# Performance work log

Hardware: AMD Instinct MI355X
Metric: run time of the kernel (lower is better)

## Reference

```python
import jax, jax.numpy as jnp
import numpy as np

N, C, SUBVEC, K, DOUT, DEPTH = 16384, 64, 16, 16, 1024, 4


def setup_inputs() -> dict:
    key = jax.random.key(0)
    k1, k2, k3, k4, k5 = jax.random.split(key, 5)
    x = jax.random.normal(k1, (N, C * SUBVEC), dtype=jnp.float32)
    split_idxs = jax.random.randint(k2, (C, DEPTH), 0, SUBVEC, dtype=jnp.int32)
    split_vals = jax.random.normal(k3, (C, DEPTH, K // 2), dtype=jnp.float32)
    lookup_tables = jax.random.normal(k4, (C, K, DOUT), dtype=jnp.float32)
    bias = jax.random.normal(k5, (DOUT,), dtype=jnp.float32)
    return {"x": x, "split_idxs": split_idxs, "split_vals": split_vals,
            "lookup_tables": lookup_tables, "bias": bias}


def _encode(x_sub, split_idxs, split_vals):
    # x_sub: (n, C, subvec_len); split_idxs: (C, 4); split_vals: (C, 4, 8)
    n = x_sub.shape[0]
    c_idx = jnp.arange(C)
    enc = jnp.zeros((n, C), dtype=jnp.int32)
    for t in range(DEPTH):  # fixed tree depth 4
        xv = x_sub[:, c_idx, split_idxs[:, t]]            # (n, C) selected feature per codebook
        thresh = split_vals[c_idx[None, :], t, enc]       # (n, C) per-node threshold
        enc = 2 * enc + (xv > thresh).astype(jnp.int32)
    return enc  # values in [0, 16)


def reference(x, split_idxs, split_vals, lookup_tables, bias):
    n = x.shape[0]
    x_sub = x.reshape(n, C, SUBVEC)
    enc = _encode(x_sub, split_idxs, split_vals)           # (n, C) int32
    onehot = jax.nn.one_hot(enc, K, dtype=x.dtype)         # (n, C, K)
    out = jnp.einsum('nck,cko->no', onehot, lookup_tables) # sum over codebooks of LUT rows
    return out + bias
```

## Files before the change

kernel.cpp:

```cpp
#include <hip/hip_runtime.h>

#define NN    16384
#define CBN   64
#define SUBV  16
#define KCODE 16
#define DOUTN 1024
#define DEP   4

typedef short bf16x8 __attribute__((ext_vector_type(8)));
typedef float f32x16 __attribute__((ext_vector_type(16)));

static __device__ __forceinline__ unsigned short f2bf(float f) {
  unsigned int u = __float_as_uint(f);
  u += 0x7FFFu + ((u >> 16) & 1u);
  return (unsigned short)(u >> 16);
}

static __device__ __forceinline__ void gld16(const void* g, void* l) {
  __builtin_amdgcn_global_load_lds(
      (const __attribute__((address_space(1))) unsigned int*)g,
      (__attribute__((address_space(3))) unsigned int*)(uintptr_t)l, 16, 0, 0);
}

__global__ __launch_bounds__(256) void prep_k(
    const float* __restrict__ x, const int* __restrict__ split_idxs,
    const float* __restrict__ split_vals, const float* __restrict__ Tg,
    unsigned char* __restrict__ codes, unsigned int* __restrict__ Tswz) {
  const int t = threadIdx.x;

  if (blockIdx.x < 64) {
    const int img = blockIdx.x;
    const int g = img >> 3, ch = img & 7;
    unsigned int* dst = Tswz + (size_t)img * 8192;
    const int colq = t & 31, kp = (t >> 5) & 7;
    #pragma unroll
    for (int cl = 0; cl < 8; ++cl) {
      const float* g0 = Tg + ((size_t)((ch * 8 + cl) * KCODE + 2 * kp)) * DOUTN
                        + g * 128 + colq * 4;
      float4 r0 = *(const float4*)g0;
      float4 r1 = *(const float4*)(g0 + DOUTN);
      unsigned int pk[4] = {
        f2bf(r0.x) | ((unsigned int)f2bf(r1.x) << 16),
        f2bf(r0.y) | ((unsigned int)f2bf(r1.y) << 16),
        f2bf(r0.z) | ((unsigned int)f2bf(r1.z) << 16),
        f2bf(r0.w) | ((unsigned int)f2bf(r1.w) << 16)};
      unsigned key = (unsigned)(colq & 7) << 2;
      #pragma unroll
      for (int j = 0; j < 4; ++j)
        dst[cl * 1024 + ((((unsigned)(colq * 4 + j)) * 8 + (unsigned)kp) ^ key)]
            = pk[j];
    }
    return;
  }

  __shared__ __align__(16) float xs[8][SUBV * CBN];
  __shared__ int   sidxT[DEP * CBN];
  __shared__ float svalT[DEP * (KCODE / 2) * CBN];
  if (t < DEP * CBN) {
    int d = t >> 6, c = t & 63;
    sidxT[t] = split_idxs[c * DEP + d];
  }
  for (int i = t; i < DEP * (KCODE / 2) * CBN; i += 256) {
    int c = i & 63, de = i >> 6, d = de >> 3, e = de & 7;
    svalT[i] = split_vals[(c * DEP + d) * (KCODE / 2) + e];
  }
  const int n0 = (blockIdx.x - 64) * 8;
  const float4* xg = (const float4*)(x + (size_t)n0 * DOUTN);
  #pragma unroll
  for (int i = 0; i < 8; ++i) {
    int li = t + i * 256;
    int r = li >> 8, cpos = li & 255;
    float4 v = xg[r * 256 + cpos];
    int c = cpos >> 2, q = cpos & 3;
    *(float4*)&xs[r][c * SUBV + ((q ^ (c & 3)) << 2)] = v;
  }
  __syncthreads();
  const int c = t & 63, rg = t >> 6;
  #pragma unroll
  for (int i = 0; i < 2; ++i) {
    int nl = rg * 2 + i;
    int e = 0;
    #pragma unroll
    for (int d = 0; d < DEP; ++d) {
      int si = sidxT[d * 64 + c];
      float xv = xs[nl][c * SUBV + (((si >> 2) ^ (c & 3)) << 2) + (si & 3)];
      float th = svalT[(d * 8 + e) * 64 + c];
      e = 2 * e + (xv > th ? 1 : 0);
    }
    codes[(size_t)(n0 + nl) * CBN + c] = (unsigned char)e;
  }
}

__global__ __launch_bounds__(1024, 4) void maddness_mfma(
    const unsigned int* __restrict__ Tswz, const float* __restrict__ bias,
    const unsigned char* __restrict__ codes, float* __restrict__ out) {
  __shared__ __align__(16) unsigned int Tb[32768];

  const int t = threadIdx.x;
  const int wid = t >> 6, lane = t & 63, lrow = lane & 31, h = lane >> 5;
  const int g16 = blockIdx.x, g8 = g16 >> 1, half = g16 & 1;
  const int n0 = blockIdx.y * 1024;
  const char* img = (const char*)Tswz + (size_t)g8 * 8 * 32768;

  #pragma unroll
  for (int i = 0; i < 8; ++i) {
    int gs = wid * 8 + i;
    int ch = gs >> 4, s16 = gs & 15, cl = s16 >> 1, pc = s16 & 1;
    gld16(img + ch * 32768 + cl * 4096 + half * 2048 + pc * 1024 + lane * 16,
          (char*)Tb + gs * 1024);
  }

  f32x16 acc[2][2];
  #pragma unroll
  for (int rt = 0; rt < 2; ++rt)
    #pragma unroll
    for (int ct = 0; ct < 2; ++ct)
      #pragma unroll
      for (int e = 0; e < 16; ++e) acc[rt][ct][e] = 0.f;

  const unsigned char* crow0 = codes + (size_t)(n0 + wid * 64 + lrow) * CBN;
  const unsigned char* crow1 = crow0 + 32 * CBN;

  __syncthreads();

  #pragma unroll
  for (int ct = 0; ct < 2; ++ct) {
    const unsigned col_loc = (unsigned)(ct * 32 + lrow);
    const unsigned rb = (col_loc * 16 + (unsigned)h * 8)
                      ^ (((col_loc >> 2) & 7u) << 3);
    const unsigned short* tb0 = (const unsigned short*)Tb + rb;

    #pragma unroll
    for (int i = 0; i < 8; ++i) {
      const int ch = (wid + i) & 7;
      const unsigned long long qw0 = *(const unsigned long long*)(crow0 + ch * 8);
      const unsigned long long qw1 = *(const unsigned long long*)(crow1 + ch * 8);
      const unsigned short* tbc = tb0 + ch * 8192;

      bf16x8 bva[4], bvb[4];
      #pragma unroll
      for (int k = 0; k < 4; ++k)
        bva[k] = *(const bf16x8*)(tbc + k * 1024);

      #pragma unroll
      for (int hb = 0; hb < 2; ++hb) {
        if (hb == 0) {
          #pragma unroll
          for (int k = 0; k < 4; ++k)
            bvb[k] = *(const bf16x8*)(tbc + (4 + k) * 1024);
        }
        #pragma unroll
        for (int k = 0; k < 4; ++k) {
          const int cl = hb * 4 + k;
          const bf16x8 bv = hb ? bvb[k] : bva[k];
          #pragma unroll
          for (int rt = 0; rt < 2; ++rt) {
            const unsigned long long q = rt ? qw1 : qw0;
            int c = (int)((q >> (8 * cl)) & 255);
            int p = c >> 1;
            unsigned s = 0x3F80u << ((c & 1) << 4);
            union { unsigned int u[4]; bf16x8 v; } A;
            #pragma unroll
            for (int j = 0; j < 4; ++j) A.u[j] = (p == h * 4 + j) ? s : 0u;
            acc[rt][ct] = __builtin_amdgcn_mfma_f32_32x32x16_bf16(A.v, bv, acc[rt][ct], 0, 0, 0);
          }
        }
      }
    }
  }

  #pragma unroll
  for (int ct = 0; ct < 2; ++ct) {
    const int col = g16 * 64 + ct * 32 + lrow;
    const float bval = bias[col];
    #pragma unroll
    for (int rt = 0; rt < 2; ++rt)
      #pragma unroll
      for (int r = 0; r < 16; ++r) {
        int row = n0 + wid * 64 + rt * 32 + (r & 3) + 8 * (r >> 2) + 4 * h;
        out[(size_t)row * DOUTN + col] = acc[rt][ct][r] + bval;
      }
  }
}

extern "C" void kernel_launch(void* const* d_in, const int* in_sizes, int n_in,
                              void* d_out, int out_size, void* d_ws, size_t ws_size,
                              hipStream_t stream) {
  const float* x    = (const float*)d_in[0];
  const int*   sidx = (const int*)d_in[1];
  const float* sval = (const float*)d_in[2];
  const float* Tg   = (const float*)d_in[3];
  const float* bias = (const float*)d_in[4];
  float* out = (float*)d_out;
  unsigned char* codes = (unsigned char*)d_ws;
  unsigned int*  Tswz  = (unsigned int*)((char*)d_ws + (1 << 20));

  prep_k<<<64 + NN / 8, 256, 0, stream>>>(x, sidx, sval, Tg, codes, Tswz);
  maddness_mfma<<<dim3(16, 16), 1024, 0, stream>>>(Tswz, bias, codes, out);
}
```

Baseline: 52.51 us.

## Remap waves to 128x32 output tiles to reuse each LUT fragment across four MFMAs

Each wave previously computed a 64x64 tile (2 row tiles x 2 column tiles), loading its B fragments from LDS twice, once per column tile. Now each wave owns a 128-row by 32-column tile, loads each bf16 LUT fragment once, and reuses it across four row tiles. This halves the LDS reads of B per wave, at the cost of four code-row global loads per chunk instead of two. Each output store now covers one 32-wide column instead of two.

After: 59.48 us. 1.13x slower.

```diff
diff --git a/kernel.cpp b/kernel.cpp
--- a/kernel.cpp
+++ b/kernel.cpp
@@ -98,6 +98,7 @@
 
   const int t = threadIdx.x;
   const int wid = t >> 6, lane = t & 63, lrow = lane & 31, h = lane >> 5;
+  const int rq = wid >> 1, cq = wid & 1;
   const int g16 = blockIdx.x, g8 = g16 >> 1, half = g16 & 1;
   const int n0 = blockIdx.y * 1024;
   const char* img = (const char*)Tswz + (size_t)g8 * 8 * 32768;
@@ -110,77 +111,54 @@
           (char*)Tb + gs * 1024);
   }
 
-  f32x16 acc[2][2];
+  f32x16 acc[4];
   #pragma unroll
-  for (int rt = 0; rt < 2; ++rt)
+  for (int rt = 0; rt < 4; ++rt)
     #pragma unroll
-    for (int ct = 0; ct < 2; ++ct)
-      #pragma unroll
-      for (int e = 0; e < 16; ++e) acc[rt][ct][e] = 0.f;
+    for (int e = 0; e < 16; ++e) acc[rt][e] = 0.f;
 
-  const unsigned char* crow0 = codes + (size_t)(n0 + wid * 64 + lrow) * CBN;
-  const unsigned char* crow1 = crow0 + 32 * CBN;
+  const unsigned char* crow = codes + (size_t)(n0 + rq * 128 + lrow) * CBN;
+
+  const unsigned col_loc = (unsigned)(cq * 32 + lrow);
+  const unsigned rb = (col_loc * 16 + (unsigned)h * 8)
+                    ^ (((col_loc >> 2) & 7u) << 3);
+  const unsigned short* tb0 = (const unsigned short*)Tb + rb;
 
   __syncthreads();
 
   #pragma unroll
-  for (int ct = 0; ct < 2; ++ct) {
-    const unsigned col_loc = (unsigned)(ct * 32 + lrow);
-    const unsigned rb = (col_loc * 16 + (unsigned)h * 8)
-                      ^ (((col_loc >> 2) & 7u) << 3);
-    const unsigned short* tb0 = (const unsigned short*)Tb + rb;
-
+  for (int i = 0; i < 8; ++i) {
+    const int ch = (wid + i) & 7;
+    unsigned long long qw[4];
     #pragma unroll
-    for (int i = 0; i < 8; ++i) {
-      const int ch = (wid + i) & 7;
-      const unsigned long long qw0 = *(const unsigned long long*)(crow0 + ch * 8);
-      const unsigned long long qw1 = *(const unsigned long long*)(crow1 + ch * 8);
-      const unsigned short* tbc = tb0 + ch * 8192;
-
-      bf16x8 bva[4], bvb[4];
+    for (int rt = 0; rt < 4; ++rt)
+      qw[rt] = *(const unsigned long long*)(crow + (size_t)rt * 32 * CBN + ch * 8);
+    const unsigned short* tbc = tb0 + ch * 8192;
+    #pragma unroll
+    for (int cl = 0; cl < 8; ++cl) {
+      const bf16x8 bv = *(const bf16x8*)(tbc + cl * 1024);
       #pragma unroll
-      for (int k = 0; k < 4; ++k)
-        bva[k] = *(const bf16x8*)(tbc + k * 1024);
-
-      #pragma unroll
-      for (int hb = 0; hb < 2; ++hb) {
-        if (hb == 0) {
-          #pragma unroll
-          for (int k = 0; k < 4; ++k)
-            bvb[k] = *(const bf16x8*)(tbc + (4 + k) * 1024);
-        }
+      for (int rt = 0; rt < 4; ++rt) {
+        int c = (int)((qw[rt] >> (8 * cl)) & 255);
+        int p = c >> 1;
+        unsigned s = 0x3F80u << ((c & 1) << 4);
+        union { unsigned int u[4]; bf16x8 v; } A;
         #pragma unroll
-        for (int k = 0; k < 4; ++k) {
-          const int cl = hb * 4 + k;
-          const bf16x8 bv = hb ? bvb[k] : bva[k];
-          #pragma unroll
-          for (int rt = 0; rt < 2; ++rt) {
-            const unsigned long long q = rt ? qw1 : qw0;
-            int c = (int)((q >> (8 * cl)) & 255);
-            int p = c >> 1;
-            unsigned s = 0x3F80u << ((c & 1) << 4);
-            union { unsigned int u[4]; bf16x8 v; } A;
-            #pragma unroll
-            for (int j = 0; j < 4; ++j) A.u[j] = (p == h * 4 + j) ? s : 0u;
-            acc[rt][ct] = __builtin_amdgcn_mfma_f32_32x32x16_bf16(A.v, bv, acc[rt][ct], 0, 0, 0);
-          }
-        }
+        for (int j = 0; j < 4; ++j) A.u[j] = (p == h * 4 + j) ? s : 0u;
+        acc[rt] = __builtin_amdgcn_mfma_f32_32x32x16_bf16(A.v, bv, acc[rt], 0, 0, 0);
       }
     }
   }
 
+  const int col = g16 * 64 + cq * 32 + lrow;
+  const float bval = bias[col];
   #pragma unroll
-  for (int ct = 0; ct < 2; ++ct) {
-    const int col = g16 * 64 + ct * 32 + lrow;
-    const float bval = bias[col];
+  for (int rt = 0; rt < 4; ++rt)
     #pragma unroll
-    for (int rt = 0; rt < 2; ++rt)
-      #pragma unroll
-      for (int r = 0; r < 16; ++r) {
-        int row = n0 + wid * 64 + rt * 32 + (r & 3) + 8 * (r >> 2) + 4 * h;
-        out[(size_t)row * DOUTN + col] = acc[rt][ct][r] + bval;
-      }
-  }
+    for (int r = 0; r < 16; ++r) {
+      int row = n0 + rq * 128 + rt * 32 + (r & 3) + 8 * (r >> 2) + 4 * h;
+      out[(size_t)row * DOUTN + col] = acc[rt][r] + bval;
+    }
 }
 
 extern "C" void kernel_launch(void* const* d_in, const int* in_sizes, int n_in,
```

## Quantize lookup tables to int8 with per-column scales and use i8 MFMA

Applied to the files above, without the earlier changes.

Replaces the bf16 lookup-table image and bf16 MFMA with int8-quantized tables, using a per-output-column absmax scale, and int32-accumulating 32x32x32 i8 MFMA. The scale is applied in the epilogue with an fma alongside the bias. This halves LDS footprint and table traffic and doubles K per MFMA, cutting the instruction count. Int8 quantization adds much more error than bf16 and may break tolerance. The prep kernel also gains a column-max reduction pass.

After: 46.68 us. -11.1%, faster.

```diff
diff --git a/kernel.cpp b/kernel.cpp
--- a/kernel.cpp
+++ b/kernel.cpp
@@ -7,14 +7,8 @@
 #define DOUTN 1024
 #define DEP   4
 
-typedef short bf16x8 __attribute__((ext_vector_type(8)));
-typedef float f32x16 __attribute__((ext_vector_type(16)));
-
-static __device__ __forceinline__ unsigned short f2bf(float f) {
-  unsigned int u = __float_as_uint(f);
-  u += 0x7FFFu + ((u >> 16) & 1u);
-  return (unsigned short)(u >> 16);
-}
+typedef int   i32x4  __attribute__((ext_vector_type(4)));
+typedef int   i32x16 __attribute__((ext_vector_type(16)));
 
 static __device__ __forceinline__ void gld16(const void* g, void* l) {
   __builtin_amdgcn_global_load_lds(
@@ -25,30 +19,52 @@
 __global__ __launch_bounds__(256) void prep_k(
     const float* __restrict__ x, const int* __restrict__ split_idxs,
     const float* __restrict__ split_vals, const float* __restrict__ Tg,
-    unsigned char* __restrict__ codes, unsigned int* __restrict__ Tswz) {
+    unsigned char* __restrict__ codes, unsigned char* __restrict__ img,
+    float* __restrict__ scales) {
   const int t = threadIdx.x;
 
   if (blockIdx.x < 64) {
-    const int img = blockIdx.x;
-    const int g = img >> 3, ch = img & 7;
-    unsigned int* dst = Tswz + (size_t)img * 8192;
-    const int colq = t & 31, kp = (t >> 5) & 7;
-    #pragma unroll
-    for (int cl = 0; cl < 8; ++cl) {
-      const float* g0 = Tg + ((size_t)((ch * 8 + cl) * KCODE + 2 * kp)) * DOUTN
-                        + g * 128 + colq * 4;
-      float4 r0 = *(const float4*)g0;
-      float4 r1 = *(const float4*)(g0 + DOUTN);
-      unsigned int pk[4] = {
-        f2bf(r0.x) | ((unsigned int)f2bf(r1.x) << 16),
-        f2bf(r0.y) | ((unsigned int)f2bf(r1.y) << 16),
-        f2bf(r0.z) | ((unsigned int)f2bf(r1.z) << 16),
-        f2bf(r0.w) | ((unsigned int)f2bf(r1.w) << 16)};
-      unsigned key = (unsigned)(colq & 7) << 2;
-      #pragma unroll
-      for (int j = 0; j < 4; ++j)
-        dst[cl * 1024 + ((((unsigned)(colq * 4 + j)) * 8 + (unsigned)kp) ^ key)]
-            = pk[j];
+    __shared__ float pm[16][17];
+    __shared__ float invs[16];
+    const int col0 = blockIdx.x * 16;
+    const int j = t & 15, rg = t >> 4;
+    float m = 0.f;
+    for (int r = rg; r < 1024; r += 16)
+      m = fmaxf(m, fabsf(Tg[(size_t)r * DOUTN + col0 + j]));
+    pm[rg][j] = m;
+    __syncthreads();
+    if (t < 16) {
+      float mm = 0.f;
+      #pragma unroll
+      for (int k = 0; k < 16; ++k) mm = fmaxf(mm, pm[k][t]);
+      scales[col0 + t] = mm * (1.f / 127.f);
+      invs[t] = 127.f / mm;
+    }
+    __syncthreads();
+    #pragma unroll
+    for (int ii = 0; ii < 4; ++ii) {
+      int u = t + ii * 256;
+      int p = u >> 5, h = (u >> 4) & 1, jj = u & 15;
+      int c = 2 * p + h;
+      int col = col0 + jj;
+      const float* src = Tg + (size_t)c * KCODE * DOUTN + col;
+      const float inv = invs[jj];
+      unsigned int pk[4];
+      #pragma unroll
+      for (int q = 0; q < 4; ++q) {
+        unsigned int w = 0;
+        #pragma unroll
+        for (int b = 0; b < 4; ++b) {
+          float v = src[(size_t)(q * 4 + b) * DOUTN];
+          float r = rintf(v * inv);
+          r = fminf(127.f, fmaxf(-127.f, r));
+          w |= ((unsigned int)((int)r & 255)) << (8 * b);
+        }
+        pk[q] = w;
+      }
+      unsigned int* dst = (unsigned int*)(img + ((size_t)(col >> 6)) * 65536
+                                          + p * 2048 + h * 1024 + (col & 63) * 16);
+      dst[0] = pk[0]; dst[1] = pk[1]; dst[2] = pk[2]; dst[3] = pk[3];
     }
     return;
   }
@@ -75,10 +91,10 @@
     *(float4*)&xs[r][c * SUBV + ((q ^ (c & 3)) << 2)] = v;
   }
   __syncthreads();
-  const int c = t & 63, rg = t >> 6;
+  const int c = t & 63, rg2 = t >> 6;
   #pragma unroll
   for (int i = 0; i < 2; ++i) {
-    int nl = rg * 2 + i;
+    int nl = rg2 * 2 + i;
     int e = 0;
     #pragma unroll
     for (int d = 0; d < DEP; ++d) {
@@ -92,79 +108,66 @@
 }
 
 __global__ __launch_bounds__(1024, 4) void maddness_mfma(
-    const unsigned int* __restrict__ Tswz, const float* __restrict__ bias,
-    const unsigned char* __restrict__ codes, float* __restrict__ out) {
-  __shared__ __align__(16) unsigned int Tb[32768];
+    const unsigned char* __restrict__ img, const float* __restrict__ scales,
+    const float* __restrict__ bias, const unsigned char* __restrict__ codes,
+    float* __restrict__ out) {
+  __shared__ __align__(16) unsigned int Tb[16384];
 
   const int t = threadIdx.x;
   const int wid = t >> 6, lane = t & 63, lrow = lane & 31, h = lane >> 5;
-  const int g16 = blockIdx.x, g8 = g16 >> 1, half = g16 & 1;
+  const int g16 = blockIdx.x;
   const int n0 = blockIdx.y * 1024;
-  const char* img = (const char*)Tswz + (size_t)g8 * 8 * 32768;
-
-  #pragma unroll
-  for (int i = 0; i < 8; ++i) {
-    int gs = wid * 8 + i;
-    int ch = gs >> 4, s16 = gs & 15, cl = s16 >> 1, pc = s16 & 1;
-    gld16(img + ch * 32768 + cl * 4096 + half * 2048 + pc * 1024 + lane * 16,
-          (char*)Tb + gs * 1024);
-  }
-
-  f32x16 acc[2][2];
+  const unsigned char* img_g = img + (size_t)g16 * 65536;
+
+  #pragma unroll
+  for (int i = 0; i < 4; ++i) {
+    int gs = wid * 4 + i;
+    gld16(img_g + gs * 1024 + lane * 16, (char*)Tb + gs * 1024);
+  }
+
+  i32x16 acc[2][2];
   #pragma unroll
   for (int rt = 0; rt < 2; ++rt)
     #pragma unroll
     for (int ct = 0; ct < 2; ++ct)
       #pragma unroll
-      for (int e = 0; e < 16; ++e) acc[rt][ct][e] = 0.f;
+      for (int e = 0; e < 16; ++e) acc[rt][ct][e] = 0;
 
   const unsigned char* crow0 = codes + (size_t)(n0 + wid * 64 + lrow) * CBN;
   const unsigned char* crow1 = crow0 + 32 * CBN;
+  const char* tb = (const char*)Tb;
 
   __syncthreads();
 
-  #pragma unroll
-  for (int ct = 0; ct < 2; ++ct) {
-    const unsigned col_loc = (unsigned)(ct * 32 + lrow);
-    const unsigned rb = (col_loc * 16 + (unsigned)h * 8)
-                      ^ (((col_loc >> 2) & 7u) << 3);
-    const unsigned short* tb0 = (const unsigned short*)Tb + rb;
-
-    #pragma unroll
-    for (int i = 0; i < 8; ++i) {
-      const int ch = (wid + i) & 7;
-      const unsigned long long qw0 = *(const unsigned long long*)(crow0 + ch * 8);
-      const unsigned long long qw1 = *(const unsigned long long*)(crow1 + ch * 8);
-      const unsigned short* tbc = tb0 + ch * 8192;
-
-      bf16x8 bva[4], bvb[4];
-      #pragma unroll
-      for (int k = 0; k < 4; ++k)
-        bva[k] = *(const bf16x8*)(tbc + k * 1024);
-
-      #pragma unroll
-      for (int hb = 0; hb < 2; ++hb) {
-        if (hb == 0) {
-          #pragma unroll
-          for (int k = 0; k < 4; ++k)
-            bvb[k] = *(const bf16x8*)(tbc + (4 + k) * 1024);
-        }
-        #pragma unroll
-        for (int k = 0; k < 4; ++k) {
-          const int cl = hb * 4 + k;
-          const bf16x8 bv = hb ? bvb[k] : bva[k];
-          #pragma unroll
-          for (int rt = 0; rt < 2; ++rt) {
-            const unsigned long long q = rt ? qw1 : qw0;
-            int c = (int)((q >> (8 * cl)) & 255);
-            int p = c >> 1;
-            unsigned s = 0x3F80u << ((c & 1) << 4);
-            union { unsigned int u[4]; bf16x8 v; } A;
-            #pragma unroll
-            for (int j = 0; j < 4; ++j) A.u[j] = (p == h * 4 + j) ? s : 0u;
-            acc[rt][ct] = __builtin_amdgcn_mfma_f32_32x32x16_bf16(A.v, bv, acc[rt][ct], 0, 0, 0);
-          }
-        }
+  const int gg0 = wid & 7;
+  unsigned long long qA0 = *(const unsigned long long*)(crow0 + gg0 * 8);
+  unsigned long long qA1 = *(const unsigned long long*)(crow1 + gg0 * 8);
+
+  #pragma unroll
+  for (int g = 0; g < 8; ++g) {
+    const int gcur = (wid + g) & 7;
+    const unsigned long long q0 = qA0, q1 = qA1;
+    if (g < 7) {
+      const int ggn = (wid + g + 1) & 7;
+      qA0 = *(const unsigned long long*)(crow0 + ggn * 8);
+      qA1 = *(const unsigned long long*)(crow1 + ggn * 8);
+    }
+    #pragma unroll
+    for (int pp = 0; pp < 4; ++pp) {
+      const int p = gcur * 4 + pp;
+      const char* pb = tb + p * 2048 + h * 1024 + lrow * 16;
+      const i32x4 b0 = *(const i32x4*)pb;
+      const i32x4 b1 = *(const i32x4*)(pb + 512);
+      const unsigned sh = (unsigned)((pp * 2 + h) * 8);
+      #pragma unroll
+      for (int rt = 0; rt < 2; ++rt) {
+        const unsigned c4 = (unsigned)((rt ? q1 : q0) >> sh) & 15u;
+        const unsigned long long tt = 1ULL << ((c4 & 7u) * 8u);
+        union { unsigned long long q[2]; i32x4 v; } A;
+        A.q[0] = (c4 < 8u) ? tt : 0ULL;
+        A.q[1] = (c4 < 8u) ? 0ULL : tt;
+        acc[rt][0] = __builtin_amdgcn_mfma_i32_32x32x32_i8(A.v, b0, acc[rt][0], 0, 0, 0);
+        acc[rt][1] = __builtin_amdgcn_mfma_i32_32x32x32_i8(A.v, b1, acc[rt][1], 0, 0, 0);
       }
     }
   }
@@ -172,13 +175,14 @@
   #pragma unroll
   for (int ct = 0; ct < 2; ++ct) {
     const int col = g16 * 64 + ct * 32 + lrow;
-    const float bval = bias[col];
+    const float sc = scales[col];
+    const float bv = bias[col];
     #pragma unroll
     for (int rt = 0; rt < 2; ++rt)
       #pragma unroll
       for (int r = 0; r < 16; ++r) {
         int row = n0 + wid * 64 + rt * 32 + (r & 3) + 8 * (r >> 2) + 4 * h;
-        out[(size_t)row * DOUTN + col] = acc[rt][ct][r] + bval;
+        out[(size_t)row * DOUTN + col] = fmaf((float)acc[rt][ct][r], sc, bv);
       }
   }
 }
@@ -192,9 +196,10 @@
   const float* Tg   = (const float*)d_in[3];
   const float* bias = (const float*)d_in[4];
   float* out = (float*)d_out;
-  unsigned char* codes = (unsigned char*)d_ws;
-  unsigned int*  Tswz  = (unsigned int*)((char*)d_ws + (1 << 20));
-
-  prep_k<<<64 + NN / 8, 256, 0, stream>>>(x, sidx, sval, Tg, codes, Tswz);
-  maddness_mfma<<<dim3(16, 16), 1024, 0, stream>>>(Tswz, bias, codes, out);
-}
+  unsigned char* codes  = (unsigned char*)d_ws;
+  unsigned char* img    = (unsigned char*)d_ws + (1 << 20);
+  float*         scales = (float*)((char*)d_ws + (2 << 20));
+
+  prep_k<<<64 + NN / 8, 256, 0, stream>>>(x, sidx, sval, Tg, codes, img, scales);
+  maddness_mfma<<<dim3(16, 16), 1024, 0, stream>>>(img, scales, bias, codes, out);
+}
```
